# Optimization experiments

Hardware: AMD Instinct MI355X
Metric: run time of the kernel (lower is better)

The kernel has to match this reference:

```python
import jax, jax.numpy as jnp
import numpy as np

B, N, T, D, S = 2, 16384, 2048, 128, 384
NW, WQ, H, L, NH = 512, 32, 128, 3, 4
NTOK = 33  # len(const.tokens)


def _ln(x):
    m = x.mean(-1, keepdims=True)
    v = x.var(-1, keepdims=True)
    return (x - m) * jax.lax.rsqrt(v + 1e-5)


def setup_inputs() -> dict:
    key = jax.random.key(0)
    ks = jax.random.split(key, 24)
    sc = 0.02
    a = jax.random.normal(ks[0], (B, T, S), jnp.float32)
    q = jax.random.normal(ks[1], (B, N, D), jnp.float32)
    c = jax.random.normal(ks[2], (B, N, D), jnp.float32)
    atom_dec_bias = jax.random.normal(ks[3], (B, NW, NH, WQ, H), jnp.float32) * 0.1
    # one-hot atom->token map: ~8 atoms per token
    tok_idx = jnp.arange(N) // (N // T)
    atom_to_token = jnp.tile(jax.nn.one_hot(tok_idx, T, dtype=jnp.float32)[None], (B, 1, 1))
    atom_mask = jnp.ones((B, N), jnp.float32)
    # windowed key indices: 128-atom neighborhood centered on each 32-atom window
    starts = np.clip(np.arange(NW) * WQ + WQ // 2 - H // 2, 0, N - H)
    key_idx = jnp.asarray(starts[:, None] + np.arange(H)[None, :], jnp.int32)
    nrm = lambda k, shp: jax.random.normal(k, shp, jnp.float32) * sc
    p = {
        'a_to_q_w': nrm(ks[4], (S, D)),
        'Wq': nrm(ks[5], (L, D, D)), 'Wk': nrm(ks[6], (L, D, D)), 'Wv': nrm(ks[7], (L, D, D)),
        'Wg': nrm(ks[8], (L, D, D)), 'Wo': nrm(ks[9], (L, D, D)),
        'Wcs': nrm(ks[10], (L, D, D)), 'Wcb': nrm(ks[11], (L, D, D)), 'Wog': nrm(ks[12], (L, D, D)),
        'Wcs2': nrm(ks[13], (L, D, D)), 'Wcb2': nrm(ks[14], (L, D, D)), 'Wog2': nrm(ks[15], (L, D, D)),
        'W1': nrm(ks[16], (L, D, 2 * D)), 'W2': nrm(ks[17], (L, D, 2 * D)), 'W3': nrm(ks[18], (L, 2 * D, D)),
        'ln_g': jnp.ones((D,), jnp.float32), 'ln_b': jnp.zeros((D,), jnp.float32),
        'Wpos': nrm(ks[19], (D, 3)), 'Wres': nrm(ks[20], (D, NTOK)), 'bres': jnp.zeros((NTOK,), jnp.float32),
    }
    return dict(a=a, q=q, c=c, atom_dec_bias=atom_dec_bias, atom_to_token=atom_to_token,
                atom_mask=atom_mask, key_idx=key_idx, **p)


def reference(a, q, c, atom_dec_bias, atom_to_token, atom_mask, key_idx,
              a_to_q_w, Wq, Wk, Wv, Wg, Wo, Wcs, Wcb, Wog, Wcs2, Wcb2, Wog2,
              W1, W2, W3, ln_g, ln_b, Wpos, Wres, bres):
    Bq, Nq, Dq = q.shape
    nw, h = key_idx.shape
    wq = Nq // nw
    nh = atom_dec_bias.shape[2]
    dh = Dq // nh
    # token -> atom broadcast (dense bmm over one-hot == gather)
    q = q + jnp.einsum('bnt,btd->bnd', atom_to_token, a @ a_to_q_w)
    cn = _ln(c)
    mbias = (1.0 - atom_mask[:, key_idx])[:, :, None, None, :] * -1e9  # (B,NW,1,1,H)
    depth = Wq.shape[0]
    for l in range(depth):
        # AdaLN conditioning on c
        hcur = _ln(q) * jax.nn.sigmoid(cn @ Wcs[l]) + cn @ Wcb[l]
        qh = (hcur @ Wq[l]).reshape(Bq, nw, wq, nh, dh)
        hk = hcur[:, key_idx]  # (B,NW,H,D) gather = to_keys
        kh = (hk @ Wk[l]).reshape(Bq, nw, h, nh, dh)
        vh = (hk @ Wv[l]).reshape(Bq, nw, h, nh, dh)
        scores = jnp.einsum('bwqhd,bwkhd->bwhqk', qh, kh) / (dh ** 0.5) + atom_dec_bias + mbias
        attn = jax.nn.softmax(scores, axis=-1)
        o = jnp.einsum('bwhqk,bwkhd->bwqhd', attn, vh).reshape(Bq, Nq, Dq)
        o = jax.nn.sigmoid(hcur @ Wg[l]) * o
        q = q + jax.nn.sigmoid(cn @ Wog[l]) * (o @ Wo[l])
        # conditioned transition (SwiGLU)
        h2 = _ln(q) * jax.nn.sigmoid(cn @ Wcs2[l]) + cn @ Wcb2[l]
        ff = (jax.nn.silu(h2 @ W1[l]) * (h2 @ W2[l])) @ W3[l]
        q = q + jax.nn.sigmoid(cn @ Wog2[l]) * ff
    # atom -> residue scatter_add pooling
    tok_idx = jnp.argmax(atom_to_token, axis=-1)  # (B,N) int
    src = q * atom_mask[..., None]
    nt = atom_to_token.shape[-1]
    s_feat = jax.vmap(lambda s, i: jax.ops.segment_sum(s, i, num_segments=nt))(src, tok_idx)
    res_type = s_feat @ Wres + bres
    # LayerNorm + Linear position head
    r_update = (_ln(q) * ln_g + ln_b) @ Wpos
    return (r_update, res_type)
```

## Files before the change

kernel.cpp:

```cpp
#include <hip/hip_runtime.h>

typedef unsigned short u16;
typedef u16 u16x4 __attribute__((ext_vector_type(4)));
typedef u16 u16x8 __attribute__((ext_vector_type(8)));
typedef __bf16 bf16x8 __attribute__((ext_vector_type(8)));
typedef float f32x4 __attribute__((ext_vector_type(4)));

#define B_  2
#define N_  16384
#define T_  2048
#define D_  128
#define S_  384
#define NW_ 512
#define WQ_ 32
#define H_  128
#define L_  3
#define NH_ 4
#define NTOK_ 33
#define BN_ (B_*N_)

__device__ __forceinline__ float b2f(u16 u) {
    return __builtin_bit_cast(float, ((unsigned)u) << 16);
}
__device__ __forceinline__ u16 f2b(float f) {
    unsigned x = __builtin_bit_cast(unsigned, f);
    unsigned r = x + 0x7fffu + ((x >> 16) & 1u);
    return (u16)(r >> 16);
}
__device__ __forceinline__ float sigf(float x) { return 1.f / (1.f + __expf(-x)); }
__device__ __forceinline__ float ldin(const void* p, size_t i, int f) {
    return f ? ((const float*)p)[i] : b2f(((const u16*)p)[i]);
}

enum { M_STORE = 0, M_CBSG = 1, M_F32 = 2 };

__global__ void sentinel_k(float* out, float v) { if (threadIdx.x == 0) out[0] = v; }

__global__ __launch_bounds__(64) void detect_k(const u16* __restrict__ a, int* flag)
{
    int t = threadIdx.x;
    u16 u = a[2 * t];
    int e = (u >> 7) & 0xFF;
    bool inval = (u != 0) && (e < 96 || e > 143);
    unsigned long long m = __ballot(inval);
    if (t == 0) flag[0] = (__popcll(m) >= 6) ? 1 : 0;
}

__global__ __launch_bounds__(256) void gemm_k(
    const u16* __restrict__ A, int lda, int asrc,
    const u16* __restrict__ WT, int K,
    u16* __restrict__ C, int ldc,
    float* __restrict__ QF, int mode, const int* __restrict__ dtf)
{
    __shared__ __align__(16) char smem[36864];
    u16 (*As)[72] = (u16(*)[72])smem;
    u16 (*Bs)[72] = (u16(*)[72])(smem + 18432);

    const int tid = threadIdx.x;
    const int m0 = blockIdx.x * 128, n0 = blockIdx.y * 128;
    const int lane = tid & 63, wid = tid >> 6;
    const int wr = (wid >> 1) * 64, wc = (wid & 1) * 64;
    const int lr = lane & 15, lq = lane >> 4;
    const int af32 = (asrc == 1 && dtf) ? dtf[0] : 0;

    f32x4 zero4 = {0.f, 0.f, 0.f, 0.f};
    f32x4 acc[4][4];
#pragma unroll
    for (int i = 0; i < 4; ++i)
#pragma unroll
        for (int j = 0; j < 4; ++j) acc[i][j] = zero4;

    for (int kt = 0; kt < K; kt += 64) {
#pragma unroll
        for (int i = 0; i < 4; ++i) {
            int id = tid + i * 256;
            int r = id >> 3, c = (id & 7) * 8;
            if (af32) {
                const float* Af = (const float*)A;
                size_t ai = (size_t)(m0 + r) * lda + kt + c;
                f32x4 p0 = *(const f32x4*)&Af[ai];
                f32x4 p1 = *(const f32x4*)&Af[ai + 4];
                u16x8 t;
                t[0] = f2b(p0[0]); t[1] = f2b(p0[1]); t[2] = f2b(p0[2]); t[3] = f2b(p0[3]);
                t[4] = f2b(p1[0]); t[5] = f2b(p1[1]); t[6] = f2b(p1[2]); t[7] = f2b(p1[3]);
                *(u16x8*)&As[r][c] = t;
            } else {
                *(u16x8*)&As[r][c] = *(const u16x8*)&A[(size_t)(m0 + r) * lda + kt + c];
            }
            *(u16x8*)&Bs[r][c] = *(const u16x8*)&WT[(size_t)(n0 + r) * K + kt + c];
        }
        __syncthreads();
#pragma unroll
        for (int ks = 0; ks < 2; ++ks) {
            bf16x8 af[4], bfr[4];
#pragma unroll
            for (int t = 0; t < 4; ++t) {
                af[t]  = *(const bf16x8*)&As[wr + t * 16 + lr][ks * 32 + lq * 8];
                bfr[t] = *(const bf16x8*)&Bs[wc + t * 16 + lr][ks * 32 + lq * 8];
            }
#pragma unroll
            for (int mt = 0; mt < 4; ++mt)
#pragma unroll
                for (int nt = 0; nt < 4; ++nt)
                    acc[mt][nt] = __builtin_amdgcn_mfma_f32_16x16x32_bf16(
                        bfr[nt], af[mt], acc[mt][nt], 0, 0, 0);
        }
        __syncthreads();
    }

    const bool sig_half = (n0 >= 128);
#pragma unroll
    for (int mt = 0; mt < 4; ++mt)
#pragma unroll
        for (int nt = 0; nt < 4; ++nt) {
            int lm = wr + mt * 16 + lr;
            int lnb = wc + nt * 16 + lq * 4;
            int m = m0 + lm;
            size_t o = (size_t)m * ldc + n0 + lnb;
            f32x4 v = acc[mt][nt];
            if (mode == M_STORE) {
                u16x4 t = {f2b(v[0]), f2b(v[1]), f2b(v[2]), f2b(v[3])};
                *(u16x4*)&C[o] = t;
            } else if (mode == M_CBSG) {
                u16x4 t;
#pragma unroll
                for (int r = 0; r < 4; ++r) t[r] = f2b(sig_half ? sigf(v[r]) : v[r]);
                *(u16x4*)&C[o] = t;
            } else {
                *(f32x4*)&QF[o] = v;
            }
        }
}

__global__ __launch_bounds__(256) void fres_k(
    const u16* __restrict__ A, int lda, int asrc, int K,
    const u16* __restrict__ WT,
    const u16* __restrict__ cnb,
    const u16* __restrict__ WE, const u16* __restrict__ WS, const u16* __restrict__ WB,
    float* __restrict__ QF,
    const u16* __restrict__ WT2, u16* __restrict__ C2, int ldc2, int n2)
{
    __shared__ __align__(16) char smem[34816 + 36864 + 2048];
    u16 (*Cs)[136] = (u16(*)[136])smem;
    u16 (*Bw)[136] = (u16(*)[136])(smem + 34816);
    u16 (*As)[72]  = (u16(*)[72])(smem + 34816);
    u16 (*Bs)[72]  = (u16(*)[72])(smem + 34816 + 18432);
    u16 (*Hs)[136] = (u16(*)[136])smem;
    u16 (*Bs2)[72] = (u16(*)[72])(smem + 34816);
    float* LNp = (float*)(smem + 34816 + 36864);

    const int tid = threadIdx.x;
    const int m0 = blockIdx.x * 128;
    const int lane = tid & 63, wid = tid >> 6;
    const int wr = (wid >> 1) * 64, wc = (wid & 1) * 64;
    const int lr = lane & 15, lq = lane >> 4;
    const bool has_ln = (WS != nullptr);

    f32x4 zero4 = {0.f, 0.f, 0.f, 0.f};

#pragma unroll
    for (int i = 0; i < 8; ++i) {
        int id = tid + i * 256;
        int r = id >> 4, c = (id & 15) * 8;
        *(u16x8*)&Cs[r][c] = *(const u16x8*)&cnb[(size_t)(m0 + r) * 128 + c];
    }

    u16x4 e1q[4][4], sgq[4][4], cbq[4][4];
    const int npre = has_ln ? 3 : 1;
    for (int p = 0; p < npre; ++p) {
        const u16* Wp = (p == 0) ? WE : (p == 1 ? WS : WB);
#pragma unroll
        for (int i = 0; i < 8; ++i) {
            int id = tid + i * 256;
            int r = id >> 4, c = (id & 15) * 8;
            *(u16x8*)&Bw[r][c] = *(const u16x8*)&Wp[(size_t)r * 128 + c];
        }
        __syncthreads();
        f32x4 pacc[4][4];
#pragma unroll
        for (int i = 0; i < 4; ++i)
#pragma unroll
            for (int j = 0; j < 4; ++j) pacc[i][j] = zero4;
#pragma unroll
        for (int kk = 0; kk < 4; ++kk) {
            bf16x8 af[4], bfr[4];
#pragma unroll
            for (int t = 0; t < 4; ++t) {
                af[t]  = *(const bf16x8*)&Cs[wr + t * 16 + lr][kk * 32 + lq * 8];
                bfr[t] = *(const bf16x8*)&Bw[wc + t * 16 + lr][kk * 32 + lq * 8];
            }
#pragma unroll
            for (int mt = 0; mt < 4; ++mt)
#pragma unroll
                for (int nt = 0; nt < 4; ++nt)
                    pacc[mt][nt] = __builtin_amdgcn_mfma_f32_16x16x32_bf16(
                        bfr[nt], af[mt], pacc[mt][nt], 0, 0, 0);
        }
        __syncthreads();
#pragma unroll
        for (int mt = 0; mt < 4; ++mt)
#pragma unroll
            for (int nt = 0; nt < 4; ++nt) {
                u16x4 t;
#pragma unroll
                for (int r = 0; r < 4; ++r) {
                    float v = pacc[mt][nt][r];
                    t[r] = f2b(p == 2 ? v : sigf(v));
                }
                if (p == 0)      e1q[mt][nt] = t;
                else if (p == 1) sgq[mt][nt] = t;
                else             cbq[mt][nt] = t;
            }
    }

    f32x4 acc[4][4];
#pragma unroll
    for (int i = 0; i < 4; ++i)
#pragma unroll
        for (int j = 0; j < 4; ++j) acc[i][j] = zero4;

    for (int kt = 0; kt < K; kt += 64) {
#pragma unroll
        for (int i = 0; i < 4; ++i) {
            int id = tid + i * 256;
            int r = id >> 3, c = (id & 7) * 8;
            if (asrc == 2) {
                size_t ab = (size_t)(m0 + r) * 512 + kt + c;
                u16x8 u1 = *(const u16x8*)&A[ab];
                u16x8 u2 = *(const u16x8*)&A[ab + 256];
                u16x8 t;
#pragma unroll
                for (int j = 0; j < 8; ++j) {
                    float x = b2f(u1[j]);
                    t[j] = f2b(x * sigf(x) * b2f(u2[j]));
                }
                *(u16x8*)&As[r][c] = t;
            } else {
                *(u16x8*)&As[r][c] = *(const u16x8*)&A[(size_t)(m0 + r) * lda + kt + c];
            }
            *(u16x8*)&Bs[r][c] = *(const u16x8*)&WT[(size_t)r * K + kt + c];
        }
        __syncthreads();
#pragma unroll
        for (int ks = 0; ks < 2; ++ks) {
            bf16x8 af[4], bfr[4];
#pragma unroll
            for (int t = 0; t < 4; ++t) {
                af[t]  = *(const bf16x8*)&As[wr + t * 16 + lr][ks * 32 + lq * 8];
                bfr[t] = *(const bf16x8*)&Bs[wc + t * 16 + lr][ks * 32 + lq * 8];
            }
#pragma unroll
            for (int mt = 0; mt < 4; ++mt)
#pragma unroll
                for (int nt = 0; nt < 4; ++nt)
                    acc[mt][nt] = __builtin_amdgcn_mfma_f32_16x16x32_bf16(
                        bfr[nt], af[mt], acc[mt][nt], 0, 0, 0);
        }
        __syncthreads();
    }

    f32x4 q[4][4];
#pragma unroll
    for (int mt = 0; mt < 4; ++mt)
#pragma unroll
        for (int nt = 0; nt < 4; ++nt) {
            int m = m0 + wr + mt * 16 + lr;
            int nb = wc + nt * 16 + lq * 4;
            size_t o = (size_t)m * 128 + nb;
            f32x4 qv = *(const f32x4*)&QF[o];
            u16x4 e = e1q[mt][nt];
#pragma unroll
            for (int r = 0; r < 4; ++r) qv[r] += b2f(e[r]) * acc[mt][nt][r];
            *(f32x4*)&QF[o] = qv;
            q[mt][nt] = qv;
        }

    if (!has_ln) return;

    float s0[4], sq0[4];
#pragma unroll
    for (int mt = 0; mt < 4; ++mt) {
        float s = 0.f, sq = 0.f;
#pragma unroll
        for (int nt = 0; nt < 4; ++nt)
#pragma unroll
            for (int r = 0; r < 4; ++r) {
                float v = q[mt][nt][r];
                s += v; sq += v * v;
            }
        s  += __shfl_xor(s, 16, 64);  sq += __shfl_xor(sq, 16, 64);
        s  += __shfl_xor(s, 32, 64);  sq += __shfl_xor(sq, 32, 64);
        s0[mt] = s; sq0[mt] = sq;
    }
    if (lq == 0) {
#pragma unroll
        for (int mt = 0; mt < 4; ++mt) {
            int row = mt * 16 + lr;
            LNp[wid * 128 + row * 2 + 0] = s0[mt];
            LNp[wid * 128 + row * 2 + 1] = sq0[mt];
        }
    }
    __syncthreads();
#pragma unroll
    for (int mt = 0; mt < 4; ++mt) {
        int row = mt * 16 + lr;
        int w0 = wid & 2;
        float S  = LNp[w0 * 128 + row * 2 + 0] + LNp[(w0 + 1) * 128 + row * 2 + 0];
        float SQ = LNp[w0 * 128 + row * 2 + 1] + LNp[(w0 + 1) * 128 + row * 2 + 1];
        float mu = S * (1.f / 128.f);
        float var = SQ * (1.f / 128.f) - mu * mu;
        float inv = rsqrtf(fmaxf(var, 0.f) + 1e-5f);
        int lm = wr + mt * 16 + lr;
#pragma unroll
        for (int nt = 0; nt < 4; ++nt) {
            u16x4 sg = sgq[mt][nt], cb = cbq[mt][nt];
            u16x4 hv;
#pragma unroll
            for (int r = 0; r < 4; ++r)
                hv[r] = f2b((q[mt][nt][r] - mu) * inv * b2f(sg[r]) + b2f(cb[r]));
            *(u16x4*)&Hs[lm][wc + nt * 16 + lq * 4] = hv;
        }
    }

    for (int nc = 0; nc < n2; nc += 128) {
        f32x4 acc2[4][4];
#pragma unroll
        for (int i = 0; i < 4; ++i)
#pragma unroll
            for (int j = 0; j < 4; ++j) acc2[i][j] = zero4;
#pragma unroll
        for (int kt2 = 0; kt2 < 128; kt2 += 64) {
            __syncthreads();
#pragma unroll
            for (int i = 0; i < 4; ++i) {
                int id = tid + i * 256;
                int r = id >> 3, c = (id & 7) * 8;
                *(u16x8*)&Bs2[r][c] =
                    *(const u16x8*)&WT2[(size_t)(nc + r) * 128 + kt2 + c];
            }
            __syncthreads();
#pragma unroll
            for (int ks = 0; ks < 2; ++ks) {
                bf16x8 af[4], bfr[4];
#pragma unroll
                for (int t = 0; t < 4; ++t) {
                    af[t]  = *(const bf16x8*)&Hs[wr + t * 16 + lr][kt2 + ks * 32 + lq * 8];
                    bfr[t] = *(const bf16x8*)&Bs2[wc + t * 16 + lr][ks * 32 + lq * 8];
                }
#pragma unroll
                for (int mt = 0; mt < 4; ++mt)
#pragma unroll
                    for (int nt = 0; nt < 4; ++nt)
                        acc2[mt][nt] = __builtin_amdgcn_mfma_f32_16x16x32_bf16(
                            bfr[nt], af[mt], acc2[mt][nt], 0, 0, 0);
            }
        }
#pragma unroll
        for (int mt = 0; mt < 4; ++mt)
#pragma unroll
            for (int nt = 0; nt < 4; ++nt) {
                int m = m0 + wr + mt * 16 + lr;
                int n = nc + wc + nt * 16 + lq * 4;
                f32x4 v = acc2[mt][nt];
                u16x4 t = {f2b(v[0]), f2b(v[1]), f2b(v[2]), f2b(v[3])};
                *(u16x4*)&C2[(size_t)m * ldc2 + n] = t;
            }
    }
}

#define VSWZ(d) ((((d) >> 3) & 7) << 3)
__global__ __launch_bounds__(256) void attn_k(
    const u16* __restrict__ proj,
    const u16* __restrict__ biasbf,
    const void* __restrict__ mask,
    const int* __restrict__ key_idx,
    u16* __restrict__ o_out,
    const int* __restrict__ dtf)
{
    __shared__ __align__(16) u16 Ks[128][136];
    __shared__ __align__(16) u16 Vt[128][136];
    const int tid = threadIdx.x;
    const int b = blockIdx.x >> 9, w = blockIdx.x & 511;
    int raw = key_idx[w * 128];
    if ((unsigned)raw > (unsigned)(N_ - H_))
        raw = (int)__builtin_bit_cast(float, raw);
    const int ks0 = raw < 0 ? 0 : (raw > N_ - H_ ? N_ - H_ : raw);
    const int lane = tid & 63, h = tid >> 6;
    const int lr = lane & 15, lq = lane >> 4;
    const int hoff = h * 32;
    const int f = dtf[0];

#pragma unroll
    for (int i = 0; i < 8; ++i) {
        int id = tid + i * 256;
        int r = id >> 4, c = (id & 15) * 8;
        size_t gbase = ((size_t)(b * N_ + ks0 + r)) * 512;
        *(u16x8*)&Ks[r][c] = *(const u16x8*)&proj[gbase + 128 + c];
        u16x8 v = *(const u16x8*)&proj[gbase + 256 + c];
#pragma unroll
        for (int j = 0; j < 8; ++j) {
            int d = c + j;
            Vt[d][r ^ VSWZ(d)] = v[j];
        }
    }
    __syncthreads();

    bf16x8 aq[2];
#pragma unroll
    for (int mt = 0; mt < 2; ++mt) {
        int qa = w * 32 + mt * 16 + lr;
        aq[mt] = *(const bf16x8*)&proj[((size_t)(b * N_ + qa)) * 512 + hoff + lq * 8];
    }
    f32x4 zero4 = {0.f, 0.f, 0.f, 0.f};
    f32x4 s[2][8];
#pragma unroll
    for (int nt = 0; nt < 8; ++nt) {
        bf16x8 bk = *(const bf16x8*)&Ks[nt * 16 + lr][hoff + lq * 8];
        s[0][nt] = __builtin_amdgcn_mfma_f32_16x16x32_bf16(aq[0], bk, zero4, 0, 0, 0);
        s[1][nt] = __builtin_amdgcn_mfma_f32_16x16x32_bf16(aq[1], bk, zero4, 0, 0, 0);
    }

    const float scl = 0.17677669529663687f;
    float mb[8];
#pragma unroll
    for (int nt = 0; nt < 8; ++nt)
        mb[nt] = (1.f - ldin(mask, (size_t)b * N_ + ks0 + nt * 16 + lr, f)) * -1e9f;
    size_t bb = (((size_t)b * 512 + w) * 4 + h) * (size_t)(32 * 128);
#pragma unroll
    for (int mt = 0; mt < 2; ++mt)
#pragma unroll
        for (int nt = 0; nt < 8; ++nt)
#pragma unroll
            for (int r = 0; r < 4; ++r) {
                int qq = mt * 16 + lq * 4 + r;
                int kk = nt * 16 + lr;
                s[mt][nt][r] = s[mt][nt][r] * scl + b2f(biasbf[bb + qq * 128 + kk]) + mb[nt];
            }

#pragma unroll
    for (int mt = 0; mt < 2; ++mt)
#pragma unroll
        for (int r = 0; r < 4; ++r) {
            float mx = -3.4e38f;
#pragma unroll
            for (int nt = 0; nt < 8; ++nt) mx = fmaxf(mx, s[mt][nt][r]);
#pragma unroll
            for (int off = 1; off < 16; off <<= 1) mx = fmaxf(mx, __shfl_xor(mx, off, 64));
            float sm = 0.f;
#pragma unroll
            for (int nt = 0; nt < 8; ++nt) {
                float p = __expf(s[mt][nt][r] - mx);
                s[mt][nt][r] = p; sm += p;
            }
#pragma unroll
            for (int off = 1; off < 16; off <<= 1) sm += __shfl_xor(sm, off, 64);
            float inv = 1.f / sm;
#pragma unroll
            for (int nt = 0; nt < 8; ++nt) s[mt][nt][r] *= inv;
        }

    __syncthreads();
#pragma unroll
    for (int mt = 0; mt < 2; ++mt)
#pragma unroll
        for (int nt = 0; nt < 8; ++nt)
#pragma unroll
            for (int r = 0; r < 4; ++r)
                Ks[hoff + mt * 16 + lq * 4 + r][nt * 16 + lr] = f2b(s[mt][nt][r]);
    __syncthreads();

    f32x4 o[2][2];
    o[0][0] = zero4; o[0][1] = zero4; o[1][0] = zero4; o[1][1] = zero4;
#pragma unroll
    for (int kst = 0; kst < 4; ++kst) {
        bf16x8 ap[2], bv[2];
#pragma unroll
        for (int mt = 0; mt < 2; ++mt)
            ap[mt] = *(const bf16x8*)&Ks[hoff + mt * 16 + lr][kst * 32 + lq * 8];
#pragma unroll
        for (int nt = 0; nt < 2; ++nt) {
            int d = hoff + nt * 16 + lr;
            bv[nt] = *(const bf16x8*)&Vt[d][(kst * 32 + lq * 8) ^ VSWZ(d)];
        }
#pragma unroll
        for (int mt = 0; mt < 2; ++mt)
#pragma unroll
            for (int nt = 0; nt < 2; ++nt)
                o[mt][nt] = __builtin_amdgcn_mfma_f32_16x16x32_bf16(ap[mt], bv[nt], o[mt][nt], 0, 0, 0);
    }

#pragma unroll
    for (int mt = 0; mt < 2; ++mt)
#pragma unroll
        for (int nt = 0; nt < 2; ++nt)
#pragma unroll
            for (int r = 0; r < 4; ++r) {
                int qa = w * 32 + mt * 16 + lq * 4 + r;
                int d = hoff + nt * 16 + lr;
                size_t gi = ((size_t)(b * N_ + qa)) * 512 + 384 + d;
                float g = sigf(b2f(proj[gi]));
                o_out[((size_t)(b * N_ + qa)) * 128 + d] = f2b(g * o[mt][nt][r]);
            }
}

struct TJob { const void* base; int off; int dst; int K; int N; };
struct TJobs { TJob j[43]; };
__global__ __launch_bounds__(256) void prologue_k(
    const void* __restrict__ bias_in, u16* __restrict__ biasbf,
    const void* __restrict__ c_in, u16* __restrict__ cn,
    TJobs jobs, u16* __restrict__ wt, const int* __restrict__ dtf)
{
    __shared__ __align__(16) u16 Ls[64][72];
    int bx = blockIdx.x;
    int f = dtf[0];
    if (bx < 8192) {
        size_t i = ((size_t)bx * 256 + threadIdx.x) * 8;
        if (f) {
            const float* s = (const float*)bias_in;
            f32x4 p0 = *(const f32x4*)&s[i];
            f32x4 p1 = *(const f32x4*)&s[i + 4];
            u16x8 t;
            t[0] = f2b(p0[0]); t[1] = f2b(p0[1]); t[2] = f2b(p0[2]); t[3] = f2b(p0[3]);
            t[4] = f2b(p1[0]); t[5] = f2b(p1[1]); t[6] = f2b(p1[2]); t[7] = f2b(p1[3]);
            *(u16x8*)&biasbf[i] = t;
        } else {
            *(u16x8*)&biasbf[i] = *(const u16x8*)&((const u16*)bias_in)[i];
        }
    } else if (bx < 16384) {
        int row = (bx - 8192) * 4 + (threadIdx.x >> 6);
        int l = threadIdx.x & 63;
        size_t base = (size_t)row * 128;
        float a = ldin(c_in, base + l, f), b = ldin(c_in, base + l + 64, f);
        float s = a + b, ss = a * a + b * b;
#pragma unroll
        for (int off = 1; off < 64; off <<= 1) {
            s  += __shfl_xor(s, off, 64);
            ss += __shfl_xor(ss, off, 64);
        }
        float m = s * (1.f / 128.f);
        float v = ss * (1.f / 128.f) - m * m;
        float inv = rsqrtf(fmaxf(v, 0.f) + 1e-5f);
        cn[base + l]      = f2b((a - m) * inv);
        cn[base + l + 64] = f2b((b - m) * inv);
    } else {
        int t = bx - 16384;
        int jidx = t / 12, tidx = t - jidx * 12;
        TJob jb = jobs.j[jidx];
        int ntk = jb.K >> 6, ntn = jb.N >> 6;
        if (tidx >= ntk * ntn) return;
        int kt = (tidx % ntk) << 6;
        int nt = (tidx / ntk) << 6;
        int r = threadIdx.x >> 3, cc = (threadIdx.x & 7) * 8;
#pragma unroll
        for (int p = 0; p < 2; ++p) {
            int kl = r + p * 32;
            size_t si = (size_t)jb.off + (size_t)(kt + kl) * jb.N + nt + cc;
            u16x8 v;
            if (f) {
                const float* s = (const float*)jb.base;
                f32x4 p0 = *(const f32x4*)&s[si];
                f32x4 p1 = *(const f32x4*)&s[si + 4];
                v[0] = f2b(p0[0]); v[1] = f2b(p0[1]); v[2] = f2b(p0[2]); v[3] = f2b(p0[3]);
                v[4] = f2b(p1[0]); v[5] = f2b(p1[1]); v[6] = f2b(p1[2]); v[7] = f2b(p1[3]);
            } else {
                v = *(const u16x8*)&((const u16*)jb.base)[si];
            }
            *(u16x8*)&Ls[kl][cc] = v;
        }
        __syncthreads();
#pragma unroll
        for (int p = 0; p < 2; ++p) {
            int nl = r + p * 32;
            u16x8 w;
#pragma unroll
            for (int j = 0; j < 8; ++j) w[j] = Ls[cc + j][nl];
            *(u16x8*)&wt[(size_t)jb.dst + (size_t)(nt + nl) * jb.K + kt + cc] = w;
        }
    }
}

__global__ __launch_bounds__(256) void initq_ln_k(
    const void* __restrict__ qin, const float* __restrict__ aw,
    float* __restrict__ qf,
    const u16* __restrict__ cs0, const u16* __restrict__ cb0, int sgcbld,
    u16* __restrict__ hcur, const int* __restrict__ dtf)
{
    int an = blockIdx.x * 4 + (threadIdx.x >> 6);
    int l = threadIdx.x & 63;
    int f = dtf[0];
    int b = an >> 14, n = an & 16383, t = n >> 3;
    size_t base = (size_t)an * 128;
    size_t ab = ((size_t)b * T_ + t) * 128;
    float a0 = ldin(qin, base + l, f)      + aw[ab + l];
    float a1 = ldin(qin, base + l + 64, f) + aw[ab + l + 64];
    qf[base + l] = a0; qf[base + l + 64] = a1;
    float s = a0 + a1, ss = a0 * a0 + a1 * a1;
#pragma unroll
    for (int off = 1; off < 64; off <<= 1) {
        s  += __shfl_xor(s, off, 64);
        ss += __shfl_xor(ss, off, 64);
    }
    float m = s * (1.f / 128.f);
    float v = ss * (1.f / 128.f) - m * m;
    float inv = rsqrtf(fmaxf(v, 0.f) + 1e-5f);
    size_t sb = (size_t)an * sgcbld;
    hcur[base + l]      = f2b((a0 - m) * inv * b2f(cs0[sb + l])      + b2f(cb0[sb + l]));
    hcur[base + l + 64] = f2b((a1 - m) * inv * b2f(cs0[sb + l + 64]) + b2f(cb0[sb + l + 64]));
}

__global__ __launch_bounds__(256) void final_k(const float* __restrict__ q,
    const void* __restrict__ ln_g, const void* __restrict__ ln_b,
    const void* __restrict__ Wpos,
    const void* __restrict__ mask, const void* __restrict__ Wres,
    const void* __restrict__ bres,
    float* __restrict__ out1, float* __restrict__ out2,
    const int* __restrict__ dtf)
{
    int f = dtf[0];
    int bx = blockIdx.x;
    if (bx < 8192) {
        int row = bx * 4 + (threadIdx.x >> 6);
        int l = threadIdx.x & 63;
        size_t base = (size_t)row * 128;
        float a = q[base + l], b = q[base + l + 64];
        float s = a + b, ss = a * a + b * b;
#pragma unroll
        for (int off = 1; off < 64; off <<= 1) {
            s  += __shfl_xor(s, off, 64);
            ss += __shfl_xor(ss, off, 64);
        }
        float m = s * (1.f / 128.f);
        float v = ss * (1.f / 128.f) - m * m;
        float inv = rsqrtf(fmaxf(v, 0.f) + 1e-5f);
        float y0 = (a - m) * inv * ldin(ln_g, l, f)      + ldin(ln_b, l, f);
        float y1 = (b - m) * inv * ldin(ln_g, l + 64, f) + ldin(ln_b, l + 64, f);
        float p0 = y0 * ldin(Wpos, l * 3 + 0, f) + y1 * ldin(Wpos, (l + 64) * 3 + 0, f);
        float p1 = y0 * ldin(Wpos, l * 3 + 1, f) + y1 * ldin(Wpos, (l + 64) * 3 + 1, f);
        float p2 = y0 * ldin(Wpos, l * 3 + 2, f) + y1 * ldin(Wpos, (l + 64) * 3 + 2, f);
#pragma unroll
        for (int off = 1; off < 64; off <<= 1) {
            p0 += __shfl_xor(p0, off, 64);
            p1 += __shfl_xor(p1, off, 64);
            p2 += __shfl_xor(p2, off, 64);
        }
        if (l == 0) {
            out1[(size_t)row * 3 + 0] = p0;
            out1[(size_t)row * 3 + 1] = p1;
            out1[(size_t)row * 3 + 2] = p2;
        }
    } else {
        __shared__ float sfeat[4][128];
        int wid = threadIdx.x >> 6, l = threadIdx.x & 63;
        int tok = (bx - 8192) * 4 + wid;
        int b = tok >> 11, t = tok & 2047;
        float a0 = 0.f, a1 = 0.f;
#pragma unroll
        for (int i = 0; i < 8; ++i) {
            size_t an = (size_t)b * N_ + t * 8 + i;
            float mk = ldin(mask, an, f);
            a0 += q[an * 128 + l] * mk;
            a1 += q[an * 128 + l + 64] * mk;
        }
        sfeat[wid][l] = a0; sfeat[wid][l + 64] = a1;
        __builtin_amdgcn_s_waitcnt(0);
        if (l < NTOK_) {
            float r = ldin(bres, l, f);
            for (int d = 0; d < 128; ++d) r += sfeat[wid][d] * ldin(Wres, d * NTOK_ + l, f);
            out2[(size_t)tok * NTOK_ + l] = r;
        }
    }
}

extern "C" void kernel_launch(void* const* d_in, const int* in_sizes, int n_in,
                              void* d_out, int out_size, void* d_ws, size_t ws_size,
                              hipStream_t stream)
{
    (void)out_size;
    float* out = (float*)d_out;
    const size_t WS_NEED = 295698432;

    static const int EXP_SZ[27] = {
        1572864, 4194304, 4194304, 16777216, 67108864, 32768, 65536,
        49152, 49152, 49152, 49152, 49152, 49152,
        49152, 49152, 49152, 49152, 49152, 49152,
        98304, 98304, 98304, 128, 128, 384, 4224, 33 };
    int bad = -1;
    int ncheck = n_in < 27 ? n_in : 27;
    for (int i = 0; i < ncheck; ++i)
        if (in_sizes[i] != EXP_SZ[i]) { bad = i; break; }
    if (bad >= 0) { sentinel_k<<<1, 64, 0, stream>>>(out, 256.0f * (bad + 1)); return; }
    if (n_in < 27) { sentinel_k<<<1, 64, 0, stream>>>(out, 8192.0f); return; }
    if (ws_size < WS_NEED) { sentinel_k<<<1, 64, 0, stream>>>(out, 12288.0f); return; }

    const void* a_in    = d_in[0];
    const void* q_in    = d_in[1];
    const void* c_in    = d_in[2];
    const void* bias_in = d_in[3];
    const void* mask_in = d_in[5];
    const int*  kidx    = (const int*)d_in[6];
    const void* a2q  = d_in[7];
    const void* Wq   = d_in[8];
    const void* Wk   = d_in[9];
    const void* Wv   = d_in[10];
    const void* Wg   = d_in[11];
    const void* Wo   = d_in[12];
    const void* Wcs  = d_in[13];
    const void* Wcb  = d_in[14];
    const void* Wog  = d_in[15];
    const void* Wcs2 = d_in[16];
    const void* Wcb2 = d_in[17];
    const void* Wog2 = d_in[18];
    const void* W1   = d_in[19];
    const void* W2   = d_in[20];
    const void* W3   = d_in[21];
    const void* ln_g = d_in[22];
    const void* ln_b = d_in[23];
    const void* Wpos = d_in[24];
    const void* Wres = d_in[25];
    const void* bres = d_in[26];

    char* ws = (char*)d_ws;
    u16*   wt      = (u16*)ws;
    int*   flag    = (int*)(ws + 2088960);
    float* qf      = (float*)(ws + 2097152);
    u16*   cn      = (u16*)(ws + 18874368);
    u16*   biasbf  = (u16*)(ws + 27262976);
    u16*   cnprojS = (u16*)(ws + 60817408);
    u16*   hcur    = (u16*)(ws + 211812352);
    u16*   proj    = (u16*)(ws + 220200960);
    u16*   obuf    = (u16*)(ws + 253755392);
    u16*   u12     = (u16*)(ws + 262144000);
    float* aw      = (float*)(ws + 262144000);

    detect_k<<<1, 64, 0, stream>>>((const u16*)a_in, flag);

    TJobs jobs; int nj = 0;
    for (int l = 0; l < 3; ++l) {
        jobs.j[nj++] = {Wq,   l * 16384, l * 65536 + 0,     128, 128};
        jobs.j[nj++] = {Wk,   l * 16384, l * 65536 + 16384, 128, 128};
        jobs.j[nj++] = {Wv,   l * 16384, l * 65536 + 32768, 128, 128};
        jobs.j[nj++] = {Wg,   l * 16384, l * 65536 + 49152, 128, 128};
        jobs.j[nj++] = {Wog,  l * 16384, 229376 + l * 16384, 128, 128};
        jobs.j[nj++] = {Wcs2, l * 16384, 278528 + l * 16384, 128, 128};
        jobs.j[nj++] = {Wcb2, l * 16384, 327680 + l * 16384, 128, 128};
        jobs.j[nj++] = {Wog2, l * 16384, 376832 + l * 16384, 128, 128};
        jobs.j[nj++] = {W1,   l * 32768, 491520 + l * 65536,         128, 256};
        jobs.j[nj++] = {W2,   l * 32768, 491520 + l * 65536 + 32768, 128, 256};
        jobs.j[nj++] = {W3,   l * 32768, 688128 + l * 32768, 256, 128};
        jobs.j[nj++] = {Wo,   l * 16384, 835584 + l * 16384, 128, 128};
    }
    jobs.j[nj++] = {Wcb, 0,     196608, 128, 128};
    jobs.j[nj++] = {Wcs, 0,     212992, 128, 128};
    jobs.j[nj++] = {Wcs, 16384, 425984, 128, 128};
    jobs.j[nj++] = {Wcs, 32768, 442368, 128, 128};
    jobs.j[nj++] = {Wcb, 16384, 458752, 128, 128};
    jobs.j[nj++] = {Wcb, 32768, 475136, 128, 128};
    jobs.j[nj++] = {a2q, 0,     786432, 384, 128};

    prologue_k<<<16384 + 43 * 12, 256, 0, stream>>>(bias_in, biasbf, c_in, cn, jobs, wt, flag);
    gemm_k<<<dim3(32, 1), 256, 0, stream>>>(
        (const u16*)a_in, S_, 1, wt + 786432, S_, nullptr, D_, aw, M_F32, flag);
    gemm_k<<<dim3(256, 2), 256, 0, stream>>>(
        cn, D_, 0, wt + 196608, D_, cnprojS, 256, nullptr, M_CBSG, nullptr);
    initq_ln_k<<<8192, 256, 0, stream>>>(q_in, aw, qf,
        cnprojS + 128, cnprojS + 0, 256, hcur, flag);

    gemm_k<<<dim3(256, 4), 256, 0, stream>>>(
        hcur, D_, 0, wt + 0, D_, proj, 512, nullptr, M_STORE, nullptr);

    for (int l = 0; l < 3; ++l) {
        const u16* wt_proj_n = wt + (l + 1) * 65536;
        const u16* wt_w12  = wt + 491520 + l * 65536;
        const u16* wt_w3   = wt + 688128 + l * 32768;
        const u16* wt_wo   = wt + 835584 + l * 16384;
        const u16* wt_og   = wt + 229376 + l * 16384;
        const u16* wt_cs2  = wt + 278528 + l * 16384;
        const u16* wt_cb2  = wt + 327680 + l * 16384;
        const u16* wt_og2  = wt + 376832 + l * 16384;
        const u16* wt_cs_n = wt + 425984 + l * 16384;
        const u16* wt_cb_n = wt + 458752 + l * 16384;

        attn_k<<<1024, 256, 0, stream>>>(proj, biasbf, mask_in, kidx, obuf, flag);
        fres_k<<<256, 256, 0, stream>>>(
            obuf, D_, 0, 128, wt_wo, cn, wt_og, wt_cs2, wt_cb2, qf,
            wt_w12, u12, 512, 512);
        if (l < 2)
            fres_k<<<256, 256, 0, stream>>>(
                u12, 512, 2, 256, wt_w3, cn, wt_og2, wt_cs_n, wt_cb_n, qf,
                wt_proj_n, proj, 512, 512);
        else
            fres_k<<<256, 256, 0, stream>>>(
                u12, 512, 2, 256, wt_w3, cn, wt_og2, nullptr, nullptr, qf,
                nullptr, nullptr, 0, 0);
    }

    final_k<<<9216, 256, 0, stream>>>(qf, ln_g, ln_b, Wpos, mask_in, Wres, bres,
                                      out, out + (size_t)BN_ * 3, flag);
}
```

Before: 860.6 us.

## Fuse SwiGLU transition into the attention-output kernel, eliminating the u12 intermediate

Merges the two per-layer fres_k launches into one. The W1/W2 projection is now computed in 128-column chunks, the silu-gate product is formed in registers and shared memory, and it is immediately multiplied by a 64-column slice of W3 into a persistent accumulator, so the (N,512) u12 buffer is never written to or read from global memory. To make this work, the prologue interleaves the W1 and W2 rows so each gate/value pair lands in adjacent output columns. This trades global memory traffic and one launch for more register pressure (an extra 4x4 accumulator) and more in-kernel synchronisation, which may lower occupancy.

```diff
diff --git a/kernel.cpp b/kernel.cpp
--- a/kernel.cpp
+++ b/kernel.cpp
@@ -1,6 +1,7 @@
 #include <hip/hip_runtime.h>
 
 typedef unsigned short u16;
+typedef u16 u16x2 __attribute__((ext_vector_type(2)));
 typedef u16 u16x4 __attribute__((ext_vector_type(4)));
 typedef u16 u16x8 __attribute__((ext_vector_type(8)));
 typedef __bf16 bf16x8 __attribute__((ext_vector_type(8)));
@@ -133,42 +134,47 @@
 }
 
 __global__ __launch_bounds__(256) void fres_k(
-    const u16* __restrict__ A, int lda, int asrc, int K,
-    const u16* __restrict__ WT,
+    const u16* __restrict__ A,
     const u16* __restrict__ cnb,
-    const u16* __restrict__ WE, const u16* __restrict__ WS, const u16* __restrict__ WB,
+    const u16* __restrict__ WT1,
+    const u16* __restrict__ WEa, const u16* __restrict__ WSa, const u16* __restrict__ WBa,
+    const u16* __restrict__ W12,
+    const u16* __restrict__ W3T,
+    const u16* __restrict__ WEb, const u16* __restrict__ WSb, const u16* __restrict__ WBb,
     float* __restrict__ QF,
-    const u16* __restrict__ WT2, u16* __restrict__ C2, int ldc2, int n2)
+    const u16* __restrict__ WT4, u16* __restrict__ C4,
+    int last)
 {
-    __shared__ __align__(16) char smem[34816 + 36864 + 2048];
+    __shared__ __align__(16) char smem[73728];
     u16 (*Cs)[136] = (u16(*)[136])smem;
+    u16 (*Hs)[136] = (u16(*)[136])smem;
     u16 (*Bw)[136] = (u16(*)[136])(smem + 34816);
     u16 (*As)[72]  = (u16(*)[72])(smem + 34816);
     u16 (*Bs)[72]  = (u16(*)[72])(smem + 34816 + 18432);
-    u16 (*Hs)[136] = (u16(*)[136])smem;
     u16 (*Bs2)[72] = (u16(*)[72])(smem + 34816);
-    float* LNp = (float*)(smem + 34816 + 36864);
+    u16 (*Ut)[72]  = (u16(*)[72])(smem + 34816 + 18432);
+    float* LNp = (float*)(smem + 71680);
 
     const int tid = threadIdx.x;
     const int m0 = blockIdx.x * 128;
     const int lane = tid & 63, wid = tid >> 6;
     const int wr = (wid >> 1) * 64, wc = (wid & 1) * 64;
     const int lr = lane & 15, lq = lane >> 4;
-    const bool has_ln = (WS != nullptr);
-
     f32x4 zero4 = {0.f, 0.f, 0.f, 0.f};
 
-#pragma unroll
-    for (int i = 0; i < 8; ++i) {
-        int id = tid + i * 256;
-        int r = id >> 4, c = (id & 15) * 8;
-        *(u16x8*)&Cs[r][c] = *(const u16x8*)&cnb[(size_t)(m0 + r) * 128 + c];
-    }
-
     u16x4 e1q[4][4], sgq[4][4], cbq[4][4];
-    const int npre = has_ln ? 3 : 1;
-    for (int p = 0; p < npre; ++p) {
-        const u16* Wp = (p == 0) ? WE : (p == 1 ? WS : WB);
+    f32x4 q[4][4];
+
+    auto stage_cn = [&]() {
+#pragma unroll
+        for (int i = 0; i < 8; ++i) {
+            int id = tid + i * 256;
+            int r = id >> 4, c = (id & 15) * 8;
+            *(u16x8*)&Cs[r][c] = *(const u16x8*)&cnb[(size_t)(m0 + r) * 128 + c];
+        }
+    };
+
+    auto pregemm = [&](const u16* Wp, int dosig, u16x4 (*out)[4]) {
 #pragma unroll
         for (int i = 0; i < 8; ++i) {
             int id = tid + i * 256;
@@ -205,40 +211,93 @@
 #pragma unroll
                 for (int r = 0; r < 4; ++r) {
                     float v = pacc[mt][nt][r];
-                    t[r] = f2b(p == 2 ? v : sigf(v));
+                    t[r] = f2b(dosig ? sigf(v) : v);
                 }
-                if (p == 0)      e1q[mt][nt] = t;
-                else if (p == 1) sgq[mt][nt] = t;
-                else             cbq[mt][nt] = t;
-            }
-    }
+                out[mt][nt] = t;
+            }
+    };
+
+    auto rmw = [&](f32x4 (*ac)[4]) {
+#pragma unroll
+        for (int mt = 0; mt < 4; ++mt)
+#pragma unroll
+            for (int nt = 0; nt < 4; ++nt) {
+                int m = m0 + wr + mt * 16 + lr;
+                int nb = wc + nt * 16 + lq * 4;
+                size_t o = (size_t)m * 128 + nb;
+                f32x4 qv = *(const f32x4*)&QF[o];
+                u16x4 e = e1q[mt][nt];
+#pragma unroll
+                for (int r = 0; r < 4; ++r) qv[r] += b2f(e[r]) * ac[mt][nt][r];
+                *(f32x4*)&QF[o] = qv;
+                q[mt][nt] = qv;
+            }
+    };
+
+    auto lnmix = [&]() {
+        float s0[4], sq0[4];
+#pragma unroll
+        for (int mt = 0; mt < 4; ++mt) {
+            float s = 0.f, sq = 0.f;
+#pragma unroll
+            for (int nt = 0; nt < 4; ++nt)
+#pragma unroll
+                for (int r = 0; r < 4; ++r) {
+                    float v = q[mt][nt][r];
+                    s += v; sq += v * v;
+                }
+            s  += __shfl_xor(s, 16, 64);  sq += __shfl_xor(sq, 16, 64);
+            s  += __shfl_xor(s, 32, 64);  sq += __shfl_xor(sq, 32, 64);
+            s0[mt] = s; sq0[mt] = sq;
+        }
+        if (lq == 0) {
+#pragma unroll
+            for (int mt = 0; mt < 4; ++mt) {
+                int row = mt * 16 + lr;
+                LNp[wid * 128 + row * 2 + 0] = s0[mt];
+                LNp[wid * 128 + row * 2 + 1] = sq0[mt];
+            }
+        }
+        __syncthreads();
+#pragma unroll
+        for (int mt = 0; mt < 4; ++mt) {
+            int row = mt * 16 + lr;
+            int w0 = wid & 2;
+            float S  = LNp[w0 * 128 + row * 2 + 0] + LNp[(w0 + 1) * 128 + row * 2 + 0];
+            float SQ = LNp[w0 * 128 + row * 2 + 1] + LNp[(w0 + 1) * 128 + row * 2 + 1];
+            float mu = S * (1.f / 128.f);
+            float var = SQ * (1.f / 128.f) - mu * mu;
+            float inv = rsqrtf(fmaxf(var, 0.f) + 1e-5f);
+            int lm = wr + mt * 16 + lr;
+#pragma unroll
+            for (int nt = 0; nt < 4; ++nt) {
+                u16x4 sg = sgq[mt][nt], cb = cbq[mt][nt];
+                u16x4 hv;
+#pragma unroll
+                for (int r = 0; r < 4; ++r)
+                    hv[r] = f2b((q[mt][nt][r] - mu) * inv * b2f(sg[r]) + b2f(cb[r]));
+                *(u16x4*)&Hs[lm][wc + nt * 16 + lq * 4] = hv;
+            }
+        }
+    };
+
+    stage_cn();
+    pregemm(WEa, 1, e1q);
+    pregemm(WSa, 1, sgq);
+    pregemm(WBa, 0, cbq);
 
     f32x4 acc[4][4];
 #pragma unroll
     for (int i = 0; i < 4; ++i)
 #pragma unroll
         for (int j = 0; j < 4; ++j) acc[i][j] = zero4;
-
-    for (int kt = 0; kt < K; kt += 64) {
+    for (int kt = 0; kt < 128; kt += 64) {
 #pragma unroll
         for (int i = 0; i < 4; ++i) {
             int id = tid + i * 256;
             int r = id >> 3, c = (id & 7) * 8;
-            if (asrc == 2) {
-                size_t ab = (size_t)(m0 + r) * 512 + kt + c;
-                u16x8 u1 = *(const u16x8*)&A[ab];
-                u16x8 u2 = *(const u16x8*)&A[ab + 256];
-                u16x8 t;
-#pragma unroll
-                for (int j = 0; j < 8; ++j) {
-                    float x = b2f(u1[j]);
-                    t[j] = f2b(x * sigf(x) * b2f(u2[j]));
-                }
-                *(u16x8*)&As[r][c] = t;
-            } else {
-                *(u16x8*)&As[r][c] = *(const u16x8*)&A[(size_t)(m0 + r) * lda + kt + c];
-            }
-            *(u16x8*)&Bs[r][c] = *(const u16x8*)&WT[(size_t)r * K + kt + c];
+            *(u16x8*)&As[r][c] = *(const u16x8*)&A[(size_t)(m0 + r) * 128 + kt + c];
+            *(u16x8*)&Bs[r][c] = *(const u16x8*)&WT1[(size_t)r * 128 + kt + c];
         }
         __syncthreads();
 #pragma unroll
@@ -258,71 +317,16 @@
         }
         __syncthreads();
     }
-
-    f32x4 q[4][4];
-#pragma unroll
-    for (int mt = 0; mt < 4; ++mt)
-#pragma unroll
-        for (int nt = 0; nt < 4; ++nt) {
-            int m = m0 + wr + mt * 16 + lr;
-            int nb = wc + nt * 16 + lq * 4;
-            size_t o = (size_t)m * 128 + nb;
-            f32x4 qv = *(const f32x4*)&QF[o];
-            u16x4 e = e1q[mt][nt];
-#pragma unroll
-            for (int r = 0; r < 4; ++r) qv[r] += b2f(e[r]) * acc[mt][nt][r];
-            *(f32x4*)&QF[o] = qv;
-            q[mt][nt] = qv;
-        }
-
-    if (!has_ln) return;
-
-    float s0[4], sq0[4];
-#pragma unroll
-    for (int mt = 0; mt < 4; ++mt) {
-        float s = 0.f, sq = 0.f;
-#pragma unroll
-        for (int nt = 0; nt < 4; ++nt)
-#pragma unroll
-            for (int r = 0; r < 4; ++r) {
-                float v = q[mt][nt][r];
-                s += v; sq += v * v;
-            }
-        s  += __shfl_xor(s, 16, 64);  sq += __shfl_xor(sq, 16, 64);
-        s  += __shfl_xor(s, 32, 64);  sq += __shfl_xor(sq, 32, 64);
-        s0[mt] = s; sq0[mt] = sq;
-    }
-    if (lq == 0) {
-#pragma unroll
-        for (int mt = 0; mt < 4; ++mt) {
-            int row = mt * 16 + lr;
-            LNp[wid * 128 + row * 2 + 0] = s0[mt];
-            LNp[wid * 128 + row * 2 + 1] = sq0[mt];
-        }
-    }
-    __syncthreads();
-#pragma unroll
-    for (int mt = 0; mt < 4; ++mt) {
-        int row = mt * 16 + lr;
-        int w0 = wid & 2;
-        float S  = LNp[w0 * 128 + row * 2 + 0] + LNp[(w0 + 1) * 128 + row * 2 + 0];
-        float SQ = LNp[w0 * 128 + row * 2 + 1] + LNp[(w0 + 1) * 128 + row * 2 + 1];
-        float mu = S * (1.f / 128.f);
-        float var = SQ * (1.f / 128.f) - mu * mu;
-        float inv = rsqrtf(fmaxf(var, 0.f) + 1e-5f);
-        int lm = wr + mt * 16 + lr;
-#pragma unroll
-        for (int nt = 0; nt < 4; ++nt) {
-            u16x4 sg = sgq[mt][nt], cb = cbq[mt][nt];
-            u16x4 hv;
-#pragma unroll
-            for (int r = 0; r < 4; ++r)
-                hv[r] = f2b((q[mt][nt][r] - mu) * inv * b2f(sg[r]) + b2f(cb[r]));
-            *(u16x4*)&Hs[lm][wc + nt * 16 + lq * 4] = hv;
-        }
-    }
-
-    for (int nc = 0; nc < n2; nc += 128) {
+    rmw(acc);
+    lnmix();
+
+    f32x4 acc3[4][4];
+#pragma unroll
+    for (int i = 0; i < 4; ++i)
+#pragma unroll
+        for (int j = 0; j < 4; ++j) acc3[i][j] = zero4;
+
+    for (int ch = 0; ch < 4; ++ch) {
         f32x4 acc2[4][4];
 #pragma unroll
         for (int i = 0; i < 4; ++i)
@@ -336,7 +340,90 @@
                 int id = tid + i * 256;
                 int r = id >> 3, c = (id & 7) * 8;
                 *(u16x8*)&Bs2[r][c] =
-                    *(const u16x8*)&WT2[(size_t)(nc + r) * 128 + kt2 + c];
+                    *(const u16x8*)&W12[(size_t)(ch * 128 + r) * 128 + kt2 + c];
+            }
+            __syncthreads();
+#pragma unroll
+            for (int ks = 0; ks < 2; ++ks) {
+                bf16x8 af[4], bfr[4];
+#pragma unroll
+                for (int t = 0; t < 4; ++t) {
+                    af[t]  = *(const bf16x8*)&Hs[wr + t * 16 + lr][kt2 + ks * 32 + lq * 8];
+                    bfr[t] = *(const bf16x8*)&Bs2[wc + t * 16 + lr][ks * 32 + lq * 8];
+                }
+#pragma unroll
+                for (int mt = 0; mt < 4; ++mt)
+#pragma unroll
+                    for (int nt = 0; nt < 4; ++nt)
+                        acc2[mt][nt] = __builtin_amdgcn_mfma_f32_16x16x32_bf16(
+                            bfr[nt], af[mt], acc2[mt][nt], 0, 0, 0);
+            }
+        }
+#pragma unroll
+        for (int mt = 0; mt < 4; ++mt)
+#pragma unroll
+            for (int nt = 0; nt < 4; ++nt) {
+                f32x4 v = acc2[mt][nt];
+                float a0 = b2f(f2b(v[0])), a1 = b2f(f2b(v[1]));
+                float a2 = b2f(f2b(v[2])), a3 = b2f(f2b(v[3]));
+                u16x2 t;
+                t[0] = f2b(a0 * sigf(a0) * a1);
+                t[1] = f2b(a2 * sigf(a2) * a3);
+                int lm = wr + mt * 16 + lr;
+                int fc = (wc >> 1) + nt * 8 + lq * 2;
+                *(u16x2*)&Ut[lm][fc] = t;
+            }
+        __syncthreads();
+#pragma unroll
+        for (int i = 0; i < 4; ++i) {
+            int id = tid + i * 256;
+            int r = id >> 3, c = (id & 7) * 8;
+            *(u16x8*)&Bs2[r][c] = *(const u16x8*)&W3T[(size_t)r * 256 + ch * 64 + c];
+        }
+        __syncthreads();
+#pragma unroll
+        for (int ks = 0; ks < 2; ++ks) {
+            bf16x8 af[4], bfr[4];
+#pragma unroll
+            for (int t = 0; t < 4; ++t) {
+                af[t]  = *(const bf16x8*)&Ut[wr + t * 16 + lr][ks * 32 + lq * 8];
+                bfr[t] = *(const bf16x8*)&Bs2[wc + t * 16 + lr][ks * 32 + lq * 8];
+            }
+#pragma unroll
+            for (int mt = 0; mt < 4; ++mt)
+#pragma unroll
+                for (int nt = 0; nt < 4; ++nt)
+                    acc3[mt][nt] = __builtin_amdgcn_mfma_f32_16x16x32_bf16(
+                        bfr[nt], af[mt], acc3[mt][nt], 0, 0, 0);
+        }
+    }
+
+    __syncthreads();
+    stage_cn();
+    pregemm(WEb, 1, e1q);
+    if (!last) {
+        pregemm(WSb, 1, sgq);
+        pregemm(WBb, 0, cbq);
+    }
+    rmw(acc3);
+    if (last) return;
+    lnmix();
+
+    for (int nc = 0; nc < 512; nc += 128) {
+        f32x4 acc2[4][4];
+#pragma unroll
+        for (int i = 0; i < 4; ++i)
+#pragma unroll
+            for (int j = 0; j < 4; ++j) acc2[i][j] = zero4;
+#pragma unroll
+        for (int kt2 = 0; kt2 < 128; kt2 += 64) {
+            __syncthreads();
+#pragma unroll
+            for (int i = 0; i < 4; ++i) {
+                int id = tid + i * 256;
+                int r = id >> 3, c = (id & 7) * 8;
+                *(u16x8*)&Bs2[r][c] =
+                    *(const u16x8*)&WT4[(size_t)(nc + r) * 128 + kt2 + c];
             }
             __syncthreads();
 #pragma unroll
@@ -363,7 +450,7 @@
                 int n = nc + wc + nt * 16 + lq * 4;
                 f32x4 v = acc2[mt][nt];
                 u16x4 t = {f2b(v[0]), f2b(v[1]), f2b(v[2]), f2b(v[3])};
-                *(u16x4*)&C2[(size_t)m * ldc2 + n] = t;
+                *(u16x4*)&C4[(size_t)m * 512 + n] = t;
             }
     }
 }
@@ -503,7 +590,7 @@
             }
 }
 
-struct TJob { const void* base; int off; int dst; int K; int N; };
+struct TJob { const void* base; int off; int dst; int K; int N; int ilv; };
 struct TJobs { TJob j[43]; };
 __global__ __launch_bounds__(256) void prologue_k(
     const void* __restrict__ bias_in, u16* __restrict__ biasbf,
@@ -574,7 +661,11 @@
             u16x8 w;
 #pragma unroll
             for (int j = 0; j < 8; ++j) w[j] = Ls[cc + j][nl];
-            *(u16x8*)&wt[(size_t)jb.dst + (size_t)(nt + nl) * jb.K + kt + cc] = w;
+            int fcol = nt + nl;
+            size_t orow = jb.ilv
+                ? (size_t)(((fcol >> 6) << 7) + ((fcol & 63) << 1) + (jb.ilv - 1))
+                : (size_t)fcol;
+            *(u16x8*)&wt[(size_t)jb.dst + orow * jb.K + kt + cc] = w;
         }
     }
 }
@@ -729,33 +820,32 @@
     u16*   hcur    = (u16*)(ws + 211812352);
     u16*   proj    = (u16*)(ws + 220200960);
     u16*   obuf    = (u16*)(ws + 253755392);
-    u16*   u12     = (u16*)(ws + 262144000);
     float* aw      = (float*)(ws + 262144000);
 
     detect_k<<<1, 64, 0, stream>>>((const u16*)a_in, flag);
 
     TJobs jobs; int nj = 0;
     for (int l = 0; l < 3; ++l) {
-        jobs.j[nj++] = {Wq,   l * 16384, l * 65536 + 0,     128, 128};
-        jobs.j[nj++] = {Wk,   l * 16384, l * 65536 + 16384, 128, 128};
-        jobs.j[nj++] = {Wv,   l * 16384, l * 65536 + 32768, 128, 128};
-        jobs.j[nj++] = {Wg,   l * 16384, l * 65536 + 49152, 128, 128};
-        jobs.j[nj++] = {Wog,  l * 16384, 229376 + l * 16384, 128, 128};
-        jobs.j[nj++] = {Wcs2, l * 16384, 278528 + l * 16384, 128, 128};
-        jobs.j[nj++] = {Wcb2, l * 16384, 327680 + l * 16384, 128, 128};
-        jobs.j[nj++] = {Wog2, l * 16384, 376832 + l * 16384, 128, 128};
-        jobs.j[nj++] = {W1,   l * 32768, 491520 + l * 65536,         128, 256};
-        jobs.j[nj++] = {W2,   l * 32768, 491520 + l * 65536 + 32768, 128, 256};
-        jobs.j[nj++] = {W3,   l * 32768, 688128 + l * 32768, 256, 128};
-        jobs.j[nj++] = {Wo,   l * 16384, 835584 + l * 16384, 128, 128};
-    }
-    jobs.j[nj++] = {Wcb, 0,     196608, 128, 128};
-    jobs.j[nj++] = {Wcs, 0,     212992, 128, 128};
-    jobs.j[nj++] = {Wcs, 16384, 425984, 128, 128};
-    jobs.j[nj++] = {Wcs, 32768, 442368, 128, 128};
-    jobs.j[nj++] = {Wcb, 16384, 458752, 128, 128};
-    jobs.j[nj++] = {Wcb, 32768, 475136, 128, 128};
-    jobs.j[nj++] = {a2q, 0,     786432, 384, 128};
+        jobs.j[nj++] = {Wq,   l * 16384, l * 65536 + 0,     128, 128, 0};
+        jobs.j[nj++] = {Wk,   l * 16384, l * 65536 + 16384, 128, 128, 0};
+        jobs.j[nj++] = {Wv,   l * 16384, l * 65536 + 32768, 128, 128, 0};
+        jobs.j[nj++] = {Wg,   l * 16384, l * 65536 + 49152, 128, 128, 0};
+        jobs.j[nj++] = {Wog,  l * 16384, 229376 + l * 16384, 128, 128, 0};
+        jobs.j[nj++] = {Wcs2, l * 16384, 278528 + l * 16384, 128, 128, 0};
+        jobs.j[nj++] = {Wcb2, l * 16384, 327680 + l * 16384, 128, 128, 0};
+        jobs.j[nj++] = {Wog2, l * 16384, 376832 + l * 16384, 128, 128, 0};
+        jobs.j[nj++] = {W1,   l * 32768, 491520 + l * 65536, 128, 256, 1};
+        jobs.j[nj++] = {W2,   l * 32768, 491520 + l * 65536, 128, 256, 2};
+        jobs.j[nj++] = {W3,   l * 32768, 688128 + l * 32768, 256, 128, 0};
+        jobs.j[nj++] = {Wo,   l * 16384, 835584 + l * 16384, 128, 128, 0};
+    }
+    jobs.j[nj++] = {Wcb, 0,     196608, 128, 128, 0};
+    jobs.j[nj++] = {Wcs, 0,     212992, 128, 128, 0};
+    jobs.j[nj++] = {Wcs, 16384, 425984, 128, 128, 0};
+    jobs.j[nj++] = {Wcs, 32768, 442368, 128, 128, 0};
+    jobs.j[nj++] = {Wcb, 16384, 458752, 128, 128, 0};
+    jobs.j[nj++] = {Wcb, 32768, 475136, 128, 128, 0};
+    jobs.j[nj++] = {a2q, 0,     786432, 384, 128, 0};
 
     prologue_k<<<16384 + 43 * 12, 256, 0, stream>>>(bias_in, biasbf, c_in, cn, jobs, wt, flag);
     gemm_k<<<dim3(32, 1), 256, 0, stream>>>(
@@ -782,16 +872,11 @@
 
         attn_k<<<1024, 256, 0, stream>>>(proj, biasbf, mask_in, kidx, obuf, flag);
         fres_k<<<256, 256, 0, stream>>>(
-            obuf, D_, 0, 128, wt_wo, cn, wt_og, wt_cs2, wt_cb2, qf,
-            wt_w12, u12, 512, 512);
-        if (l < 2)
-            fres_k<<<256, 256, 0, stream>>>(
-                u12, 512, 2, 256, wt_w3, cn, wt_og2, wt_cs_n, wt_cb_n, qf,
-                wt_proj_n, proj, 512, 512);
-        else
-            fres_k<<<256, 256, 0, stream>>>(
-                u12, 512, 2, 256, wt_w3, cn, wt_og2, nullptr, nullptr, qf,
-                nullptr, nullptr, 0, 0);
+            obuf, cn, wt_wo, wt_og, wt_cs2, wt_cb2,
+            wt_w12, wt_w3, wt_og2,
+            l < 2 ? wt_cs_n : nullptr, l < 2 ? wt_cb_n : nullptr,
+            qf,
+            l < 2 ? wt_proj_n : nullptr, proj, l == 2 ? 1 : 0);
     }
 
     final_k<<<9216, 256, 0, stream>>>(qf, ln_g, ln_b, Wpos, mask_in, Wres, bres,
```

Result: faster. 806.9 us (-6.2%).
